# Kernel tuning notes

Hardware: AMD Instinct MI355X
Metric: run time of the kernel (lower is better)

## Reference

```python
import jax, jax.numpy as jnp
import numpy as np

V, N, C, DIM, DSPAN, H = 200000, 16384, 16, 300, 512, 150


def setup_inputs() -> dict:
    key = jax.random.key(0)
    ks = jax.random.split(key, 6)
    span_vecs = jax.random.normal(ks[0], (1, N, DSPAN), jnp.float32)
    candidates = jax.random.randint(ks[1], (1, N, C), 0, V)
    # binary candidate mask; guarantee every span has at least one candidate
    mask = (jax.random.uniform(ks[2], (1, N, C)) > 0.3).astype(jnp.float32)
    mask = mask.at[..., 0].set(1.0)
    embed_table = jax.random.normal(ks[3], (V, DIM), jnp.float32) * 0.1
    W1 = jax.random.normal(ks[4], (DSPAN + DIM, H), jnp.float32) * (1.0 / np.sqrt(DSPAN + DIM))
    b1 = jnp.zeros((H,), jnp.float32)
    W2 = jax.random.normal(ks[5], (H, 1), jnp.float32) * (1.0 / np.sqrt(H))
    b2 = jnp.zeros((1,), jnp.float32)
    return dict(span_vecs=span_vecs, candidates=candidates, mask_candidates=mask,
                embed_table=embed_table, W1=W1, b1=b1, W2=W2, b2=b2)


def reference(span_vecs, candidates, mask_candidates, embed_table, W1, b1, W2, b2):
    # gather candidate entity embeddings: [N, C, dim]
    cand_emb = embed_table[candidates[0]]
    sv = span_vecs[0]                                  # [N, Dspan]
    n, c = cand_emb.shape[0], cand_emb.shape[1]
    spans_exp = jnp.broadcast_to(sv[:, None, :], (n, c, sv.shape[-1]))
    ment = jnp.concatenate([spans_exp, cand_emb], axis=-1)  # [N, C, Dspan+dim]
    # 2-layer attention MLP scorer
    h = jax.nn.relu(ment @ W1 + b1)                    # [N, C, H]
    scores = (h @ W2 + b2)[..., 0]                     # [N, C]
    # masked softmax over candidates (log(0) = -inf masks out)
    scores = jax.nn.softmax(scores + jnp.log(mask_candidates[0]), axis=-1)
    # weighted sum of candidate embeddings
    weighted = jnp.einsum('ncd,nc->nd', cand_emb, scores)   # [N, dim]
    # pad span_vecs with dim zeros then scatter weighted into last dim slots
    # == concat since every span has candidates here
    out = jnp.concatenate([sv, weighted], axis=-1)[None]    # [1, N, Dspan+dim]
    return out
```

## Files before the change

### kernel.cpp

```cpp
#include <hip/hip_runtime.h>
#include <hip/hip_bf16.h>
#include <math.h>

#define NSPANS 16384
#define CC     16
#define DIM    300
#define DSPAN  512
#define HH     150
#define HP     160
#define DMENT  812
#define KP     320

typedef short bf16x8 __attribute__((ext_vector_type(8)));
typedef float f32x4  __attribute__((ext_vector_type(4)));

__device__ __forceinline__ unsigned short f2bf(float f) {
    union { float f; unsigned int u; } v; v.f = f;
    unsigned int r = (v.u + 0x7FFFu + ((v.u >> 16) & 1u)) >> 16;
    return (unsigned short)r;
}

__global__ __launch_bounds__(256) void k0_prep(const float* __restrict__ W1,
                                               unsigned short* __restrict__ Wt) {
    int idx = blockIdx.x * 256 + threadIdx.x;
    int n = idx / KP, k = idx - n * KP;
    float v = (n < HH && k < DIM) ? W1[(size_t)(DSPAN + k) * HH + n] : 0.f;
    Wt[idx] = f2bf(v);
}

__global__ __launch_bounds__(256) void k1_span(const float* __restrict__ sv,
                                               const float* __restrict__ W1,
                                               const float* __restrict__ b1,
                                               float* __restrict__ out) {
    const int b  = blockIdx.x;
    const int t  = threadIdx.x;
    const int n0 = b * 16;

    __shared__ float svc[16][36];
    __shared__ float w1c[32][HP];

    #pragma unroll
    for (int i = 0; i < 8; ++i) {
        int idx4 = t + i * 256;
        int r    = idx4 >> 7;
        int c4   = idx4 & 127;
        float4 v = *(const float4*)(sv + (size_t)(n0 + r) * DSPAN + c4 * 4);
        *(float4*)(out + (size_t)(n0 + r) * DMENT + c4 * 4) = v;
    }

    const int tc = t & 15;
    const int tr = t >> 4;
    const int j0 = tc * 10;

    float acc[10];
    #pragma unroll
    for (int j = 0; j < 10; ++j) acc[j] = 0.f;

    for (int k0 = 0; k0 < DSPAN; k0 += 32) {
        __syncthreads();
        {
            int idx = t * 2;
            int r = idx >> 5, kk = idx & 31;
            float2 v = *(const float2*)(sv + (size_t)(n0 + r) * DSPAN + k0 + kk);
            svc[r][kk]     = v.x;
            svc[r][kk + 1] = v.y;
        }
        #pragma unroll
        for (int i = 0; i < 20; ++i) {
            int idx = t + i * 256;
            int k = idx / HP, j = idx % HP;
            w1c[k][j] = (j < HH) ? W1[(size_t)(k0 + k) * HH + j] : 0.f;
        }
        __syncthreads();
        #pragma unroll
        for (int kk = 0; kk < 32; ++kk) {
            float a = svc[tr][kk];
            #pragma unroll
            for (int j = 0; j < 10; ++j)
                acc[j] += a * w1c[kk][j0 + j];
        }
    }

    #pragma unroll
    for (int j = 0; j < 10; ++j) {
        int jj = j0 + j;
        if (jj < HH)
            out[(size_t)(n0 + tr) * DMENT + DSPAN + jj] = acc[j] + b1[jj];
    }
}

__global__ __launch_bounds__(256) void k2_mfma(const int*   __restrict__ cand,
                                               const float* __restrict__ mask,
                                               const float* __restrict__ emb,
                                               const unsigned short* __restrict__ Wt,
                                               const float* __restrict__ W2,
                                               float*       __restrict__ out) {
    const int b  = blockIdx.x;
    const int t  = threadIdx.x;
    const int n0 = b * 4;
    const int w  = t >> 6;
    const int l  = t & 63;
    const int sp = l & 15;
    const int g  = l >> 4;

    __shared__ unsigned short A_lds[64][72];
    __shared__ unsigned short B_lds[160][72];
    __shared__ float hsL[4][HP];
    __shared__ float w2L[HP];
    __shared__ int   candL[64];
    __shared__ float maskL[64];
    __shared__ float scoresL[64];
    __shared__ float pL[64];

    if (t < 64) {
        candL[t] = cand[n0 * CC + t];
        maskL[t] = mask[n0 * CC + t];
    }
    #pragma unroll
    for (int i = 0; i < 3; ++i) {
        int idx = t + i * 256;
        if (idx < 4 * HP) {
            int s = idx / HP, j = idx - s * HP;
            hsL[s][j] = (j < HH) ? out[(size_t)(n0 + s) * DMENT + DSPAN + j] : 0.f;
        }
    }
    if (t < HP) w2L[t] = (t < HH) ? W2[t] : 0.f;
    __syncthreads();

    f32x4 acc[10];
    #pragma unroll
    for (int i = 0; i < 10; ++i) acc[i] = 0.f;

    for (int k0 = 0; k0 < KP; k0 += 64) {
        __syncthreads();
        {
            int r = t >> 2, q = t & 3;
            int base = k0 + q * 16;
            const float* src = emb + (size_t)candL[r] * DIM + base;
            unsigned short tmp[16];
            if (base + 16 <= DIM) {
                #pragma unroll
                for (int i2 = 0; i2 < 4; ++i2) {
                    float4 v = *(const float4*)(src + i2 * 4);
                    tmp[i2 * 4 + 0] = f2bf(v.x);
                    tmp[i2 * 4 + 1] = f2bf(v.y);
                    tmp[i2 * 4 + 2] = f2bf(v.z);
                    tmp[i2 * 4 + 3] = f2bf(v.w);
                }
            } else {
                #pragma unroll
                for (int i2 = 0; i2 < 16; ++i2) {
                    int kg = base + i2;
                    tmp[i2] = (kg < DIM) ? f2bf(src[i2]) : (unsigned short)0;
                }
            }
            uint4 p0, p1;
            p0.x = tmp[0]  | (tmp[1]  << 16);
            p0.y = tmp[2]  | (tmp[3]  << 16);
            p0.z = tmp[4]  | (tmp[5]  << 16);
            p0.w = tmp[6]  | (tmp[7]  << 16);
            p1.x = tmp[8]  | (tmp[9]  << 16);
            p1.y = tmp[10] | (tmp[11] << 16);
            p1.z = tmp[12] | (tmp[13] << 16);
            p1.w = tmp[14] | (tmp[15] << 16);
            *(uint4*)&A_lds[r][q * 16]     = p0;
            *(uint4*)&A_lds[r][q * 16 + 8] = p1;
        }
        #pragma unroll
        for (int i2 = 0; i2 < 5; ++i2) {
            int idx = t + i2 * 256;
            int row = idx >> 3, seg = idx & 7;
            uint4 v = *(const uint4*)(Wt + (size_t)row * KP + k0 + seg * 8);
            *(uint4*)&B_lds[row][seg * 8] = v;
        }
        __syncthreads();
        #pragma unroll
        for (int ks = 0; ks < 2; ++ks) {
            int koff = ks * 32 + g * 8;
            bf16x8 af = *(const bf16x8*)&A_lds[w * 16 + sp][koff];
            #pragma unroll
            for (int nt = 0; nt < 10; ++nt) {
                bf16x8 bfr = *(const bf16x8*)&B_lds[nt * 16 + sp][koff];
                acc[nt] = __builtin_amdgcn_mfma_f32_16x16x32_bf16(af, bfr, acc[nt], 0, 0, 0);
            }
        }
    }

    float part0 = 0.f, part1 = 0.f, part2 = 0.f, part3 = 0.f;
    #pragma unroll
    for (int nt = 0; nt < 10; ++nt) {
        int col = nt * 16 + sp;
        float hb  = hsL[w][col];
        float w2v = w2L[col];
        part0 += fmaxf(acc[nt][0] + hb, 0.f) * w2v;
        part1 += fmaxf(acc[nt][1] + hb, 0.f) * w2v;
        part2 += fmaxf(acc[nt][2] + hb, 0.f) * w2v;
        part3 += fmaxf(acc[nt][3] + hb, 0.f) * w2v;
    }
    #pragma unroll
    for (int m = 1; m < 16; m <<= 1) {
        part0 += __shfl_xor(part0, m, 64);
        part1 += __shfl_xor(part1, m, 64);
        part2 += __shfl_xor(part2, m, 64);
        part3 += __shfl_xor(part3, m, 64);
    }
    if (sp == 0) {
        scoresL[w * 16 + g * 4 + 0] = part0;
        scoresL[w * 16 + g * 4 + 1] = part1;
        scoresL[w * 16 + g * 4 + 2] = part2;
        scoresL[w * 16 + g * 4 + 3] = part3;
    }
    __syncthreads();

    if (t < 64) {
        float v = (maskL[t] > 0.f) ? scoresL[t] : -INFINITY;
        float mx = v;
        #pragma unroll
        for (int m = 1; m < 16; m <<= 1) mx = fmaxf(mx, __shfl_xor(mx, m, 64));
        float e = expf(v - mx);
        float sm = e;
        #pragma unroll
        for (int m = 1; m < 16; m <<= 1) sm += __shfl_xor(sm, m, 64);
        pL[t] = e / sm;
    }
    __syncthreads();

    for (int idx = t; idx < 4 * DIM; idx += 256) {
        int s = idx / DIM, d = idx - s * DIM;
        float a = 0.f;
        #pragma unroll
        for (int c = 0; c < CC; ++c)
            a += pL[s * CC + c] * emb[(size_t)candL[s * CC + c] * DIM + d];
        out[(size_t)(n0 + s) * DMENT + DSPAN + d] = a;
    }
}

extern "C" void kernel_launch(void* const* d_in, const int* in_sizes, int n_in,
                              void* d_out, int out_size, void* d_ws, size_t ws_size,
                              hipStream_t stream) {
    const float* sv   = (const float*)d_in[0];
    const int*   cand = (const int*)d_in[1];
    const float* mask = (const float*)d_in[2];
    const float* emb  = (const float*)d_in[3];
    const float* W1   = (const float*)d_in[4];
    const float* b1   = (const float*)d_in[5];
    const float* W2   = (const float*)d_in[6];
    float* out = (float*)d_out;
    unsigned short* Wt = (unsigned short*)d_ws;

    k0_prep<<<(HP * KP) / 256, 256, 0, stream>>>(W1, Wt);
    k1_span<<<NSPANS / 16, 256, 0, stream>>>(sv, W1, b1, out);
    k2_mfma<<<NSPANS / 4, 256, 0, stream>>>(cand, mask, emb, Wt, W2, out);
}
```

Baseline: 721.5 us.

## Enlarge per-block tiles in span GEMM and MFMA scorer to reuse weight tiles

After: 659.3 us. -8.6%, faster.

```diff
diff --git a/kernel.cpp b/kernel.cpp
--- a/kernel.cpp
+++ b/kernel.cpp
@@ -34,59 +34,69 @@
                                                float* __restrict__ out) {
     const int b  = blockIdx.x;
     const int t  = threadIdx.x;
-    const int n0 = b * 16;
-
-    __shared__ float svc[16][36];
+    const int n0 = b * 32;
+
+    __shared__ float svc_t[32][36];
     __shared__ float w1c[32][HP];
 
     #pragma unroll
-    for (int i = 0; i < 8; ++i) {
+    for (int i = 0; i < 16; ++i) {
         int idx4 = t + i * 256;
-        int r    = idx4 >> 7;
-        int c4   = idx4 & 127;
+        int r = idx4 >> 7, c4 = idx4 & 127;
         float4 v = *(const float4*)(sv + (size_t)(n0 + r) * DSPAN + c4 * 4);
         *(float4*)(out + (size_t)(n0 + r) * DMENT + c4 * 4) = v;
     }
 
-    const int tc = t & 15;
-    const int tr = t >> 4;
-    const int j0 = tc * 10;
-
-    float acc[10];
-    #pragma unroll
-    for (int j = 0; j < 10; ++j) acc[j] = 0.f;
+    const int tc = t & 31;
+    const int tr = t >> 5;
+    const int j0 = tc * 5;
+    const int r0 = tr * 4;
+
+    float acc[4][5];
+    #pragma unroll
+    for (int i = 0; i < 4; ++i)
+        #pragma unroll
+        for (int j = 0; j < 5; ++j) acc[i][j] = 0.f;
 
     for (int k0 = 0; k0 < DSPAN; k0 += 32) {
         __syncthreads();
         {
-            int idx = t * 2;
-            int r = idx >> 5, kk = idx & 31;
-            float2 v = *(const float2*)(sv + (size_t)(n0 + r) * DSPAN + k0 + kk);
-            svc[r][kk]     = v.x;
-            svc[r][kk + 1] = v.y;
+            int r = t >> 3, c4 = t & 7;
+            float4 v = *(const float4*)(sv + (size_t)(n0 + r) * DSPAN + k0 + c4 * 4);
+            svc_t[c4 * 4 + 0][r] = v.x;
+            svc_t[c4 * 4 + 1][r] = v.y;
+            svc_t[c4 * 4 + 2][r] = v.z;
+            svc_t[c4 * 4 + 3][r] = v.w;
         }
         #pragma unroll
         for (int i = 0; i < 20; ++i) {
             int idx = t + i * 256;
-            int k = idx / HP, j = idx % HP;
+            int k = idx / HP, j = idx - (idx / HP) * HP;
             w1c[k][j] = (j < HH) ? W1[(size_t)(k0 + k) * HH + j] : 0.f;
         }
         __syncthreads();
         #pragma unroll
         for (int kk = 0; kk < 32; ++kk) {
-            float a = svc[tr][kk];
-            #pragma unroll
-            for (int j = 0; j < 10; ++j)
-                acc[j] += a * w1c[kk][j0 + j];
-        }
-    }
-
-    #pragma unroll
-    for (int j = 0; j < 10; ++j) {
-        int jj = j0 + j;
-        if (jj < HH)
-            out[(size_t)(n0 + tr) * DMENT + DSPAN + jj] = acc[j] + b1[jj];
-    }
+            float4 a4 = *(const float4*)&svc_t[kk][r0];
+            #pragma unroll
+            for (int j = 0; j < 5; ++j) {
+                float w = w1c[kk][j0 + j];
+                acc[0][j] += a4.x * w;
+                acc[1][j] += a4.y * w;
+                acc[2][j] += a4.z * w;
+                acc[3][j] += a4.w * w;
+            }
+        }
+    }
+
+    #pragma unroll
+    for (int i = 0; i < 4; ++i)
+        #pragma unroll
+        for (int j = 0; j < 5; ++j) {
+            int jj = j0 + j;
+            if (jj < HH)
+                out[(size_t)(n0 + r0 + i) * DMENT + DSPAN + jj] = acc[i][j] + b1[jj];
+        }
 }
 
 __global__ __launch_bounds__(256) void k2_mfma(const int*   __restrict__ cand,
@@ -97,74 +107,70 @@
                                                float*       __restrict__ out) {
     const int b  = blockIdx.x;
     const int t  = threadIdx.x;
-    const int n0 = b * 4;
+    const int n0 = b * 16;
     const int w  = t >> 6;
     const int l  = t & 63;
     const int sp = l & 15;
     const int g  = l >> 4;
 
-    __shared__ unsigned short A_lds[64][72];
+    __shared__ unsigned short A_lds[256][72];
     __shared__ unsigned short B_lds[160][72];
-    __shared__ float hsL[4][HP];
+    __shared__ float hsL[16][HP];
     __shared__ float w2L[HP];
-    __shared__ int   candL[64];
-    __shared__ float maskL[64];
-    __shared__ float scoresL[64];
-    __shared__ float pL[64];
-
-    if (t < 64) {
-        candL[t] = cand[n0 * CC + t];
-        maskL[t] = mask[n0 * CC + t];
-    }
-    #pragma unroll
-    for (int i = 0; i < 3; ++i) {
+    __shared__ int   candL[256];
+    __shared__ float maskL[256];
+    __shared__ float scoresL[256];
+    __shared__ float pL[256];
+
+    candL[t] = cand[n0 * CC + t];
+    maskL[t] = mask[n0 * CC + t];
+    #pragma unroll
+    for (int i = 0; i < 10; ++i) {
         int idx = t + i * 256;
-        if (idx < 4 * HP) {
-            int s = idx / HP, j = idx - s * HP;
-            hsL[s][j] = (j < HH) ? out[(size_t)(n0 + s) * DMENT + DSPAN + j] : 0.f;
-        }
+        int s = idx / HP, j = idx - (idx / HP) * HP;
+        hsL[s][j] = (j < HH) ? out[(size_t)(n0 + s) * DMENT + DSPAN + j] : 0.f;
     }
     if (t < HP) w2L[t] = (t < HH) ? W2[t] : 0.f;
     __syncthreads();
 
-    f32x4 acc[10];
-    #pragma unroll
-    for (int i = 0; i < 10; ++i) acc[i] = 0.f;
+    const float* asrc = emb + (size_t)candL[t] * DIM;
+
+    f32x4 acc[4][10];
+    #pragma unroll
+    for (int rt = 0; rt < 4; ++rt)
+        #pragma unroll
+        for (int nt = 0; nt < 10; ++nt) acc[rt][nt] = 0.f;
 
     for (int k0 = 0; k0 < KP; k0 += 64) {
         __syncthreads();
-        {
-            int r = t >> 2, q = t & 3;
-            int base = k0 + q * 16;
-            const float* src = emb + (size_t)candL[r] * DIM + base;
-            unsigned short tmp[16];
-            if (base + 16 <= DIM) {
+        if (k0 + 64 <= DIM) {
+            #pragma unroll
+            for (int q = 0; q < 8; ++q) {
+                float4 v0 = *(const float4*)(asrc + k0 + q * 8);
+                float4 v1 = *(const float4*)(asrc + k0 + q * 8 + 4);
+                uint4 p;
+                p.x = f2bf(v0.x) | ((unsigned)f2bf(v0.y) << 16);
+                p.y = f2bf(v0.z) | ((unsigned)f2bf(v0.w) << 16);
+                p.z = f2bf(v1.x) | ((unsigned)f2bf(v1.y) << 16);
+                p.w = f2bf(v1.z) | ((unsigned)f2bf(v1.w) << 16);
+                *(uint4*)&A_lds[t][q * 8] = p;
+            }
+        } else {
+            #pragma unroll
+            for (int q = 0; q < 8; ++q) {
+                unsigned short e[8];
                 #pragma unroll
-                for (int i2 = 0; i2 < 4; ++i2) {
-                    float4 v = *(const float4*)(src + i2 * 4);
-                    tmp[i2 * 4 + 0] = f2bf(v.x);
-                    tmp[i2 * 4 + 1] = f2bf(v.y);
-                    tmp[i2 * 4 + 2] = f2bf(v.z);
-                    tmp[i2 * 4 + 3] = f2bf(v.w);
+                for (int i2 = 0; i2 < 8; ++i2) {
+                    int kg = k0 + q * 8 + i2;
+                    e[i2] = (kg < DIM) ? f2bf(asrc[kg]) : (unsigned short)0;
                 }
-            } else {
-                #pragma unroll
-                for (int i2 = 0; i2 < 16; ++i2) {
-                    int kg = base + i2;
-                    tmp[i2] = (kg < DIM) ? f2bf(src[i2]) : (unsigned short)0;
-                }
-            }
-            uint4 p0, p1;
-            p0.x = tmp[0]  | (tmp[1]  << 16);
-            p0.y = tmp[2]  | (tmp[3]  << 16);
-            p0.z = tmp[4]  | (tmp[5]  << 16);
-            p0.w = tmp[6]  | (tmp[7]  << 16);
-            p1.x = tmp[8]  | (tmp[9]  << 16);
-            p1.y = tmp[10] | (tmp[11] << 16);
-            p1.z = tmp[12] | (tmp[13] << 16);
-            p1.w = tmp[14] | (tmp[15] << 16);
-            *(uint4*)&A_lds[r][q * 16]     = p0;
-            *(uint4*)&A_lds[r][q * 16 + 8] = p1;
+                uint4 p;
+                p.x = e[0] | ((unsigned)e[1] << 16);
+                p.y = e[2] | ((unsigned)e[3] << 16);
+                p.z = e[4] | ((unsigned)e[5] << 16);
+                p.w = e[6] | ((unsigned)e[7] << 16);
+                *(uint4*)&A_lds[t][q * 8] = p;
+            }
         }
         #pragma unroll
         for (int i2 = 0; i2 < 5; ++i2) {
@@ -177,42 +183,51 @@
         #pragma unroll
         for (int ks = 0; ks < 2; ++ks) {
             int koff = ks * 32 + g * 8;
-            bf16x8 af = *(const bf16x8*)&A_lds[w * 16 + sp][koff];
+            bf16x8 af[4];
+            #pragma unroll
+            for (int rt = 0; rt < 4; ++rt)
+                af[rt] = *(const bf16x8*)&A_lds[w * 64 + rt * 16 + sp][koff];
             #pragma unroll
             for (int nt = 0; nt < 10; ++nt) {
                 bf16x8 bfr = *(const bf16x8*)&B_lds[nt * 16 + sp][koff];
-                acc[nt] = __builtin_amdgcn_mfma_f32_16x16x32_bf16(af, bfr, acc[nt], 0, 0, 0);
-            }
-        }
-    }
-
-    float part0 = 0.f, part1 = 0.f, part2 = 0.f, part3 = 0.f;
-    #pragma unroll
-    for (int nt = 0; nt < 10; ++nt) {
-        int col = nt * 16 + sp;
-        float hb  = hsL[w][col];
-        float w2v = w2L[col];
-        part0 += fmaxf(acc[nt][0] + hb, 0.f) * w2v;
-        part1 += fmaxf(acc[nt][1] + hb, 0.f) * w2v;
-        part2 += fmaxf(acc[nt][2] + hb, 0.f) * w2v;
-        part3 += fmaxf(acc[nt][3] + hb, 0.f) * w2v;
-    }
-    #pragma unroll
-    for (int m = 1; m < 16; m <<= 1) {
-        part0 += __shfl_xor(part0, m, 64);
-        part1 += __shfl_xor(part1, m, 64);
-        part2 += __shfl_xor(part2, m, 64);
-        part3 += __shfl_xor(part3, m, 64);
-    }
-    if (sp == 0) {
-        scoresL[w * 16 + g * 4 + 0] = part0;
-        scoresL[w * 16 + g * 4 + 1] = part1;
-        scoresL[w * 16 + g * 4 + 2] = part2;
-        scoresL[w * 16 + g * 4 + 3] = part3;
+                #pragma unroll
+                for (int rt = 0; rt < 4; ++rt)
+                    acc[rt][nt] = __builtin_amdgcn_mfma_f32_16x16x32_bf16(af[rt], bfr, acc[rt][nt], 0, 0, 0);
+            }
+        }
+    }
+
+    #pragma unroll
+    for (int rt = 0; rt < 4; ++rt) {
+        int s = 4 * w + rt;
+        float p0 = 0.f, p1 = 0.f, p2 = 0.f, p3 = 0.f;
+        #pragma unroll
+        for (int nt = 0; nt < 10; ++nt) {
+            int col = nt * 16 + sp;
+            float hb  = hsL[s][col];
+            float w2v = w2L[col];
+            p0 += fmaxf(acc[rt][nt][0] + hb, 0.f) * w2v;
+            p1 += fmaxf(acc[rt][nt][1] + hb, 0.f) * w2v;
+            p2 += fmaxf(acc[rt][nt][2] + hb, 0.f) * w2v;
+            p3 += fmaxf(acc[rt][nt][3] + hb, 0.f) * w2v;
+        }
+        #pragma unroll
+        for (int m = 1; m < 16; m <<= 1) {
+            p0 += __shfl_xor(p0, m, 64);
+            p1 += __shfl_xor(p1, m, 64);
+            p2 += __shfl_xor(p2, m, 64);
+            p3 += __shfl_xor(p3, m, 64);
+        }
+        if (sp == 0) {
+            scoresL[s * 16 + g * 4 + 0] = p0;
+            scoresL[s * 16 + g * 4 + 1] = p1;
+            scoresL[s * 16 + g * 4 + 2] = p2;
+            scoresL[s * 16 + g * 4 + 3] = p3;
+        }
     }
     __syncthreads();
 
-    if (t < 64) {
+    {
         float v = (maskL[t] > 0.f) ? scoresL[t] : -INFINITY;
         float mx = v;
         #pragma unroll
@@ -225,13 +240,16 @@
     }
     __syncthreads();
 
-    for (int idx = t; idx < 4 * DIM; idx += 256) {
-        int s = idx / DIM, d = idx - s * DIM;
-        float a = 0.f;
-        #pragma unroll
-        for (int c = 0; c < CC; ++c)
-            a += pL[s * CC + c] * emb[(size_t)candL[s * CC + c] * DIM + d];
-        out[(size_t)(n0 + s) * DMENT + DSPAN + d] = a;
+    for (int idx = t; idx < 16 * 75; idx += 256) {
+        int s = idx / 75, q = idx - s * 75;
+        float4 a = make_float4(0.f, 0.f, 0.f, 0.f);
+        #pragma unroll
+        for (int c = 0; c < CC; ++c) {
+            float p = pL[s * CC + c];
+            float4 v = *(const float4*)(emb + (size_t)candL[s * CC + c] * DIM + q * 4);
+            a.x += p * v.x; a.y += p * v.y; a.z += p * v.z; a.w += p * v.w;
+        }
+        *(float4*)(out + (size_t)(n0 + s) * DMENT + DSPAN + q * 4) = a;
     }
 }
 
@@ -249,6 +267,6 @@
     unsigned short* Wt = (unsigned short*)d_ws;
 
     k0_prep<<<(HP * KP) / 256, 256, 0, stream>>>(W1, Wt);
-    k1_span<<<NSPANS / 16, 256, 0, stream>>>(sv, W1, b1, out);
-    k2_mfma<<<NSPANS / 4, 256, 0, stream>>>(cand, mask, emb, Wt, W2, out);
-}
+    k1_span<<<NSPANS / 32, 256, 0, stream>>>(sv, W1, b1, out);
+    k2_mfma<<<NSPANS / 16, 256, 0, stream>>>(cand, mask, emb, Wt, W2, out);
+}
```
